# Kernel optimization log

Hardware: AMD Instinct MI355X
Metric: run time of the kernel (lower is better)

The kernel has to match this reference:

```python
import jax, jax.numpy as jnp
import numpy as np

N_NODES = 50000
N_EDGES = 800000


def _inv_sqrt_deg(idx, n):
    deg = jax.ops.segment_sum(jnp.ones(idx.shape, jnp.float32), idx, num_segments=n)
    return jnp.where(deg > 0, deg ** -0.5, 0.0)


def graph_conv(x, W, b, src, dst, norm_src, norm_dst):
    # DGL GraphConv, norm='both': D_dst^{-1/2} A D_src^{-1/2} X W + b
    # Apply weight before aggregation (out_feats < in_feats in both layers).
    h = (x * norm_src[:, None]) @ W            # [N, out]
    m = h[src]                                  # gather per-edge messages [E, out]
    agg = jax.ops.segment_sum(m, dst, num_segments=x.shape[0])
    return agg * norm_dst[:, None] + b


def setup_inputs() -> dict:
    key = jax.random.key(0)
    ks = jax.random.split(key, 6)
    x = jax.random.normal(ks[0], (N_NODES, 512), jnp.float32)
    W1 = jax.random.normal(ks[1], (512, 128), jnp.float32) * (512 ** -0.5)
    b1 = jnp.zeros((128,), jnp.float32)
    W2 = jax.random.normal(ks[2], (128, 40), jnp.float32) * (128 ** -0.5)
    b2 = jnp.zeros((40,), jnp.float32)
    src = jax.random.randint(ks[3], (N_EDGES,), 0, N_NODES, jnp.int32)
    dst = jax.random.randint(ks[4], (N_EDGES,), 0, N_NODES, jnp.int32)
    return {"x": x, "W1": W1, "b1": b1, "W2": W2, "b2": b2, "src": src, "dst": dst}


def reference(x, W1, b1, W2, b2, src, dst):
    n = x.shape[0]
    norm_src = _inv_sqrt_deg(src, n)  # out-degree based src norm
    norm_dst = _inv_sqrt_deg(dst, n)  # in-degree based dst norm
    h = graph_conv(x, W1, b1, src, dst, norm_src, norm_dst)
    h = jax.nn.relu(h)
    h = graph_conv(h, W2, b2, src, dst, norm_src, norm_dst)
    return h
```

## Files before the change

kernel.cpp:

```cpp
#include <hip/hip_runtime.h>
#include <hip/hip_bf16.h>

#define F0 512
#define F1 128
#define F2 40

#define NRP 12800
#define G_SL 64

typedef __attribute__((ext_vector_type(8))) short bf16x8;
typedef __attribute__((ext_vector_type(4))) float f32x4;

__device__ inline ushort f2bf(float f) {
    union { float f; uint u; } v; v.f = f;
    uint u = v.u;
    uint r = u + 0x7fffu + ((u >> 16) & 1u);
    return (ushort)(r >> 16);
}
__device__ inline float bf2f(ushort h) {
    union { uint u; float f; } v; v.u = ((uint)h) << 16;
    return v.f;
}

__global__ __launch_bounds__(1024)
void hist_kernel(const int* __restrict__ src, const int* __restrict__ dst,
                 ushort* __restrict__ Gsrc, ushort* __restrict__ Gdst, int n, int E) {
    __shared__ uint cs[NRP / 2];
    __shared__ uint cd[NRP / 2];
    const int p = blockIdx.x / G_SL;
    const int g = blockIdx.x % G_SL;
    const int base = p * NRP;
    for (int i = threadIdx.x; i < NRP / 2; i += 1024) { cs[i] = 0; cd[i] = 0; }
    __syncthreads();
    const int Epg = (E + G_SL - 1) / G_SL;
    const int e0 = g * Epg;
    const int e1 = min(E, e0 + Epg);
    for (int i = e0 + (int)threadIdx.x; i < e1; i += 1024) {
        int s = src[i], d = dst[i];
        unsigned so = (unsigned)(s - base);
        unsigned dd = (unsigned)(d - base);
        if (so < (unsigned)NRP) atomicAdd(&cs[so >> 1], 1u << ((so & 1) * 16));
        if (dd < (unsigned)NRP) atomicAdd(&cd[dd >> 1], 1u << ((dd & 1) * 16));
    }
    __syncthreads();
    const int lim = min(NRP, n - base);
    for (int i = threadIdx.x; i < lim; i += 1024) {
        uint pcs = cs[i >> 1], pcd = cd[i >> 1];
        int sh = (i & 1) * 16;
        Gsrc[(size_t)g * n + base + i] = (ushort)((pcs >> sh) & 0xffffu);
        Gdst[(size_t)g * n + base + i] = (ushort)((pcd >> sh) & 0xffffu);
    }
}

__global__ __launch_bounds__(256)
void scanA_kernel(const ushort* __restrict__ Gsrc, const ushort* __restrict__ Gdst,
                  float* __restrict__ norm_src, float* __restrict__ norm_dst,
                  int* __restrict__ row_off, int* __restrict__ bsum, int n) {
    __shared__ int sm[256];
    int i = blockIdx.x * 256 + threadIdx.x;
    int s = 0, d = 0;
    if (i < n) {
#pragma unroll
        for (int g = 0; g < G_SL; g++) {
            s += Gsrc[(size_t)g * n + i];
            d += Gdst[(size_t)g * n + i];
        }
        norm_src[i] = s > 0 ? rsqrtf((float)s) : 0.f;
        norm_dst[i] = d > 0 ? rsqrtf((float)d) : 0.f;
    }
    sm[threadIdx.x] = (i < n) ? d : 0;
    __syncthreads();
    for (int off = 1; off < 256; off <<= 1) {
        int t = (threadIdx.x >= (unsigned)off) ? sm[threadIdx.x - off] : 0;
        __syncthreads();
        sm[threadIdx.x] += t;
        __syncthreads();
    }
    if (i < n) row_off[i + 1] = sm[threadIdx.x];
    if (threadIdx.x == 255) bsum[blockIdx.x] = sm[255];
}

__global__ __launch_bounds__(256)
void finalize_kernel(int* __restrict__ row_off, const int* __restrict__ bsum,
                     const ushort* __restrict__ Gdst, int* __restrict__ Goff, int n) {
    __shared__ int sm[256];
    const int b = blockIdx.x;
    const int t = threadIdx.x;
    sm[t] = (t < b) ? bsum[t] : 0;
    __syncthreads();
#pragma unroll
    for (int off = 128; off > 0; off >>= 1) {
        if (t < off) sm[t] += sm[t + off];
        __syncthreads();
    }
    const int excl = sm[0];
    const int v = b * 256 + t;
    if (v >= n) return;
    int raw = row_off[v];
    int start = excl + ((t == 0) ? 0 : raw);
    if (v == n - 1) {
        int rawn = row_off[n];
        row_off[n] = excl + rawn;
    }
    row_off[v] = start;
    int run = start;
#pragma unroll
    for (int g = 0; g < G_SL; g++) {
        size_t idx = (size_t)g * n + v;
        Goff[idx] = run;
        run += Gdst[idx];
    }
}

__global__ __launch_bounds__(1024)
void place_kernel(const int* __restrict__ src, const int* __restrict__ dst,
                  const int* __restrict__ Goff, int* __restrict__ edge_src, int n, int E) {
    __shared__ int cur[NRP];
    const int p = blockIdx.x / G_SL;
    const int g = blockIdx.x % G_SL;
    const int base = p * NRP;
    const int lim = min(NRP, n - base);
    for (int i = threadIdx.x; i < lim; i += 1024)
        cur[i] = Goff[(size_t)g * n + base + i];
    __syncthreads();
    const int Epg = (E + G_SL - 1) / G_SL;
    const int e0 = g * Epg;
    const int e1 = min(E, e0 + Epg);
    for (int i = e0 + (int)threadIdx.x; i < e1; i += 1024) {
        int d = dst[i];
        unsigned dd = (unsigned)(d - base);
        if (dd < (unsigned)lim) {
            int pos = atomicAdd(&cur[dd], 1);
            edge_src[pos] = src[i];
        }
    }
}

__global__ __launch_bounds__(256)
void wconv1_kernel(const float* __restrict__ W1, ushort* __restrict__ Wt_hi) {
    int idx = blockIdx.x * 256 + threadIdx.x;
    int k = idx >> 7, nn = idx & 127;
    Wt_hi[nn * F0 + k] = f2bf(W1[idx]);
}

#define BM 64
__global__ __launch_bounds__(256)
void gemm1_mfma(const float* __restrict__ x, const ushort* __restrict__ Wt_hi,
                const float* __restrict__ norm_src, ushort* __restrict__ h1g, int n) {
    __shared__ __align__(16) ushort Al[2][4][2][64][8];

    const int tid = threadIdx.x;
    const int lane = tid & 63;
    const int w = tid >> 6;
    const int l15 = lane & 15;
    const int lq = lane >> 4;
    const int bm = blockIdx.x * BM;

    const int smi = tid >> 6;
    const int sflane = tid & 63;
    const int srow = smi * 16 + (tid & 15);
    const int skc = (tid >> 4) & 3;
    const int grow = bm + srow;
    const bool arok = grow < n;
    const float* xrow = x + (size_t)(arok ? grow : 0) * F0 + skc * 8;

    const size_t bgoff0 = (size_t)((w * 2 + 0) * 16 + l15) * F0 + lq * 8;
    const size_t bgoff1 = (size_t)((w * 2 + 1) * 16 + l15) * F0 + lq * 8;

    f32x4 acc[4][2] = {};
    float4 a0, a1;
    bf16x8 bcur0, bcur1, bnxt0, bnxt1;

    auto loadA = [&](int k0) {
        if (arok) {
            a0 = *reinterpret_cast<const float4*>(xrow + k0);
            a1 = *reinterpret_cast<const float4*>(xrow + k0 + 4);
        } else {
            a0 = make_float4(0.f, 0.f, 0.f, 0.f);
            a1 = a0;
        }
    };
    auto stageA = [&](int buf) {
        float cf[8] = {a0.x, a0.y, a0.z, a0.w, a1.x, a1.y, a1.z, a1.w};
        uint hu[4], lu[4];
#pragma unroll
        for (int j = 0; j < 4; j++) {
            float fa = cf[2 * j], fb = cf[2 * j + 1];
            __hip_bfloat162 h2 = __float22bfloat162_rn(make_float2(fa, fb));
            uint h; __builtin_memcpy(&h, &h2, 4);
            float ra = __uint_as_float(h << 16);
            float rb = __uint_as_float(h & 0xffff0000u);
            __hip_bfloat162 l2 = __float22bfloat162_rn(make_float2(fa - ra, fb - rb));
            uint l; __builtin_memcpy(&l, &l2, 4);
            hu[j] = h; lu[j] = l;
        }
        *reinterpret_cast<uint4*>(&Al[buf][smi][0][sflane][0]) = make_uint4(hu[0], hu[1], hu[2], hu[3]);
        *reinterpret_cast<uint4*>(&Al[buf][smi][1][sflane][0]) = make_uint4(lu[0], lu[1], lu[2], lu[3]);
    };
    auto compute = [&](int buf, bf16x8 b0, bf16x8 b1) {
#pragma unroll
        for (int mi = 0; mi < 4; mi++) {
            bf16x8 ah = *reinterpret_cast<const bf16x8*>(&Al[buf][mi][0][lane][0]);
            bf16x8 al = *reinterpret_cast<const bf16x8*>(&Al[buf][mi][1][lane][0]);
            acc[mi][0] = __builtin_amdgcn_mfma_f32_16x16x32_bf16(ah, b0, acc[mi][0], 0, 0, 0);
            acc[mi][0] = __builtin_amdgcn_mfma_f32_16x16x32_bf16(al, b0, acc[mi][0], 0, 0, 0);
            acc[mi][1] = __builtin_amdgcn_mfma_f32_16x16x32_bf16(ah, b1, acc[mi][1], 0, 0, 0);
            acc[mi][1] = __builtin_amdgcn_mfma_f32_16x16x32_bf16(al, b1, acc[mi][1], 0, 0, 0);
        }
    };

    loadA(0);
    bcur0 = *reinterpret_cast<const bf16x8*>(Wt_hi + bgoff0);
    bcur1 = *reinterpret_cast<const bf16x8*>(Wt_hi + bgoff1);
    stageA(0);
    __syncthreads();

    for (int kt = 0; kt < 16; kt++) {
        const int cb = kt & 1;
        if (kt < 15) {
            loadA((kt + 1) * 32);
            bnxt0 = *reinterpret_cast<const bf16x8*>(Wt_hi + bgoff0 + (kt + 1) * 32);
            bnxt1 = *reinterpret_cast<const bf16x8*>(Wt_hi + bgoff1 + (kt + 1) * 32);
        }
        compute(cb, bcur0, bcur1);
        if (kt < 15) {
            stageA(cb ^ 1);
            bcur0 = bnxt0; bcur1 = bnxt1;
            __syncthreads();
        }
    }

#pragma unroll
    for (int mi = 0; mi < 4; mi++) {
        int rbase = bm + mi * 16 + lq * 4;
#pragma unroll
        for (int r = 0; r < 4; r++) {
            int row = rbase + r;
            if (row < n) {
                float ns = norm_src[row];
#pragma unroll
                for (int ni = 0; ni < 2; ni++) {
                    h1g[(size_t)row * F1 + w * 32 + ni * 16 + l15] = f2bf(acc[mi][ni][r] * ns);
                }
            }
        }
    }
}

__global__ __launch_bounds__(256)
void agg1_kernel(const ushort* __restrict__ h1g, const int* __restrict__ row_off,
                 const int* __restrict__ edge_src, const float* __restrict__ norm_dst,
                 const float* __restrict__ b1, ushort* __restrict__ h1, int n) {
    int wid = (blockIdx.x * blockDim.x + threadIdx.x) >> 6;
    int lane = threadIdx.x & 63;
    if (wid >= n) return;
    int beg = row_off[wid], end = row_off[wid + 1];
    float a0 = 0.f, a1 = 0.f;
    int e = beg;
    for (; e + 3 < end; e += 4) {
        int s0 = edge_src[e + 0];
        int s1 = edge_src[e + 1];
        int s2 = edge_src[e + 2];
        int s3 = edge_src[e + 3];
        uint v0 = *reinterpret_cast<const uint*>(&h1g[(size_t)s0 * F1 + lane * 2]);
        uint v1 = *reinterpret_cast<const uint*>(&h1g[(size_t)s1 * F1 + lane * 2]);
        uint v2 = *reinterpret_cast<const uint*>(&h1g[(size_t)s2 * F1 + lane * 2]);
        uint v3 = *reinterpret_cast<const uint*>(&h1g[(size_t)s3 * F1 + lane * 2]);
        a0 += (__uint_as_float(v0 << 16) + __uint_as_float(v1 << 16)) +
              (__uint_as_float(v2 << 16) + __uint_as_float(v3 << 16));
        a1 += (__uint_as_float(v0 & 0xffff0000u) + __uint_as_float(v1 & 0xffff0000u)) +
              (__uint_as_float(v2 & 0xffff0000u) + __uint_as_float(v3 & 0xffff0000u));
    }
    for (; e < end; ++e) {
        int s = edge_src[e];
        uint v = *reinterpret_cast<const uint*>(&h1g[(size_t)s * F1 + lane * 2]);
        a0 += __uint_as_float(v << 16);
        a1 += __uint_as_float(v & 0xffff0000u);
    }
    float nd = norm_dst[wid];
    float o0 = fmaxf(a0 * nd + b1[lane * 2 + 0], 0.f);
    float o1 = fmaxf(a1 * nd + b1[lane * 2 + 1], 0.f);
    __hip_bfloat162 p2 = __float22bfloat162_rn(make_float2(o0, o1));
    uint pu; __builtin_memcpy(&pu, &p2, 4);
    *reinterpret_cast<uint*>(&h1[(size_t)wid * F1 + lane * 2]) = pu;
}

__global__ __launch_bounds__(256)
void gemm2_kernel(const ushort* __restrict__ h1, const float* __restrict__ W2,
                  const float* __restrict__ norm_src, ushort* __restrict__ h2g, int n) {
    __shared__ __align__(16) float W2s[F1][F2];
    for (int i = threadIdx.x; i < F1 * F2; i += 256)
        W2s[i / F2][i % F2] = W2[i];
    __syncthreads();
    int node = blockIdx.x * 256 + threadIdx.x;
    if (node >= n) return;
    float nrm = norm_src[node];
    f32x4 acc4[10] = {};
    const ushort* row = &h1[(size_t)node * F1];
    for (int kc = 0; kc < 16; kc++) {
        uint4 u = *reinterpret_cast<const uint4*>(&row[kc * 8]);
        uint uu[4] = {u.x, u.y, u.z, u.w};
        float f[8];
#pragma unroll
        for (int i = 0; i < 4; i++) {
            f[2 * i + 0] = __uint_as_float(uu[i] << 16);
            f[2 * i + 1] = __uint_as_float(uu[i] & 0xffff0000u);
        }
#pragma unroll
        for (int j = 0; j < 8; j++) {
#pragma unroll
            for (int c4 = 0; c4 < 10; c4++) {
                f32x4 wv = *reinterpret_cast<const f32x4*>(&W2s[kc * 8 + j][c4 * 4]);
                acc4[c4] += f[j] * wv;
            }
        }
    }
    ushort* orow = &h2g[(size_t)node * F2];
#pragma unroll
    for (int c4 = 0; c4 < 10; c4++) {
        f32x4 o = acc4[c4] * nrm;
        __hip_bfloat162 pa = __float22bfloat162_rn(make_float2(o[0], o[1]));
        __hip_bfloat162 pb = __float22bfloat162_rn(make_float2(o[2], o[3]));
        uint2 pk;
        __builtin_memcpy(&pk.x, &pa, 4);
        __builtin_memcpy(&pk.y, &pb, 4);
        *reinterpret_cast<uint2*>(&orow[c4 * 4]) = pk;
    }
}

__global__ __launch_bounds__(256)
void agg2_kernel(const ushort* __restrict__ h2g, const int* __restrict__ row_off,
                 const int* __restrict__ edge_src, const float* __restrict__ norm_dst,
                 const float* __restrict__ b2, float* __restrict__ out, int n) {
    int wid = (blockIdx.x * blockDim.x + threadIdx.x) >> 6;
    int lane = threadIdx.x & 63;
    if (wid >= n) return;
    int beg = row_off[wid], end = row_off[wid + 1];
    float a0 = 0.f, a1 = 0.f, b0 = 0.f, b1v = 0.f;
    int e = beg;
    const bool act = lane < 20;
    for (; e + 3 < end; e += 4) {
        int s0 = edge_src[e + 0];
        int s1 = edge_src[e + 1];
        int s2 = edge_src[e + 2];
        int s3 = edge_src[e + 3];
        if (act) {
            uint v0 = *reinterpret_cast<const uint*>(&h2g[(size_t)s0 * F2 + lane * 2]);
            uint v1 = *reinterpret_cast<const uint*>(&h2g[(size_t)s1 * F2 + lane * 2]);
            uint v2 = *reinterpret_cast<const uint*>(&h2g[(size_t)s2 * F2 + lane * 2]);
            uint v3 = *reinterpret_cast<const uint*>(&h2g[(size_t)s3 * F2 + lane * 2]);
            a0 += (__uint_as_float(v0 << 16) + __uint_as_float(v1 << 16)) +
                  (__uint_as_float(v2 << 16) + __uint_as_float(v3 << 16));
            b0 += (__uint_as_float(v0 & 0xffff0000u) + __uint_as_float(v1 & 0xffff0000u)) +
                  (__uint_as_float(v2 & 0xffff0000u) + __uint_as_float(v3 & 0xffff0000u));
        }
    }
    for (; e < end; ++e) {
        int s = edge_src[e];
        if (act) {
            uint v = *reinterpret_cast<const uint*>(&h2g[(size_t)s * F2 + lane * 2]);
            a1 += __uint_as_float(v << 16);
            b1v += __uint_as_float(v & 0xffff0000u);
        }
    }
    if (act) {
        float nd = norm_dst[wid];
        float o0 = (a0 + a1) * nd + b2[lane * 2 + 0];
        float o1 = (b0 + b1v) * nd + b2[lane * 2 + 1];
        *reinterpret_cast<float2*>(&out[(size_t)wid * F2 + lane * 2]) = make_float2(o0, o1);
    }
}

extern "C" void kernel_launch(void* const* d_in, const int* in_sizes, int n_in,
                              void* d_out, int out_size, void* d_ws, size_t ws_size,
                              hipStream_t stream) {
    const float* x  = (const float*)d_in[0];
    const float* W1 = (const float*)d_in[1];
    const float* b1 = (const float*)d_in[2];
    const float* W2 = (const float*)d_in[3];
    const float* b2 = (const float*)d_in[4];
    const int* src  = (const int*)d_in[5];
    const int* dst  = (const int*)d_in[6];
    float* out = (float*)d_out;

    const int n = in_sizes[0] / F0;
    const int E = in_sizes[5];
    const int nb = (n + 255) / 256;
    const int P = (n + NRP - 1) / NRP;

    char* ws = (char*)d_ws;
    auto alloc = [&](size_t bytes) -> char* {
        char* p = ws;
        ws += (bytes + 255) & ~(size_t)255;
        return p;
    };
    int* row_off   = (int*)alloc((size_t)(n + 1) * 4);
    int* bsum      = (int*)alloc(256 * 4);
    int* edge_srcs = (int*)alloc((size_t)E * 4);
    float* norm_src_d = (float*)alloc((size_t)n * 4);
    float* norm_dst_d = (float*)alloc((size_t)n * 4);
    ushort* W1t_hi = (ushort*)alloc((size_t)F1 * F0 * 2);
    ushort* h1g = (ushort*)alloc((size_t)n * F1 * 2);
    ushort* h1  = (ushort*)alloc((size_t)n * F1 * 2);
    ushort* h2g = h1g;

    ushort* Gsrc = (ushort*)h1g;
    ushort* Gdst = Gsrc + (size_t)G_SL * n;
    int* Goff = (int*)h1;

    hist_kernel<<<P * G_SL, 1024, 0, stream>>>(src, dst, Gsrc, Gdst, n, E);
    scanA_kernel<<<nb, 256, 0, stream>>>(Gsrc, Gdst, norm_src_d, norm_dst_d, row_off, bsum, n);
    finalize_kernel<<<nb, 256, 0, stream>>>(row_off, bsum, Gdst, Goff, n);
    place_kernel<<<P * G_SL, 1024, 0, stream>>>(src, dst, Goff, edge_srcs, n, E);
    wconv1_kernel<<<(F0 * F1) / 256, 256, 0, stream>>>(W1, W1t_hi);
    gemm1_mfma<<<(n + BM - 1) / BM, 256, 0, stream>>>(x, W1t_hi, norm_src_d, h1g, n);
    agg1_kernel<<<(n + 3) / 4, 256, 0, stream>>>(h1g, row_off, edge_srcs, norm_dst_d, b1, h1, n);
    gemm2_kernel<<<(n + 255) / 256, 256, 0, stream>>>(h1, W2, norm_src_d, h2g, n);
    agg2_kernel<<<(n + 3) / 4, 256, 0, stream>>>(h2g, row_off, edge_srcs, norm_dst_d, b2, out, n);
}
```

Before: 195.0 us.

## Drop split-bf16 GEMM1, fuse W1 convert into histogram, deepen prefetch and gather unroll

```diff
diff --git a/kernel.cpp b/kernel.cpp
--- a/kernel.cpp
+++ b/kernel.cpp
@@ -17,14 +17,16 @@
     uint r = u + 0x7fffu + ((u >> 16) & 1u);
     return (ushort)(r >> 16);
 }
-__device__ inline float bf2f(ushort h) {
-    union { uint u; float f; } v; v.u = ((uint)h) << 16;
-    return v.f;
-}
 
 __global__ __launch_bounds__(1024)
 void hist_kernel(const int* __restrict__ src, const int* __restrict__ dst,
-                 ushort* __restrict__ Gsrc, ushort* __restrict__ Gdst, int n, int E) {
+                 ushort* __restrict__ Gsrc, ushort* __restrict__ Gdst,
+                 const float* __restrict__ W1, ushort* __restrict__ Wt, int n, int E) {
+    if (blockIdx.x < (F0 * F1) / 1024) {
+        int idx = blockIdx.x * 1024 + threadIdx.x;
+        int k = idx >> 7, nn = idx & 127;
+        Wt[nn * F0 + k] = f2bf(W1[idx]);
+    }
     __shared__ uint cs[NRP / 2];
     __shared__ uint cd[NRP / 2];
     const int p = blockIdx.x / G_SL;
@@ -136,18 +138,11 @@
     }
 }
 
-__global__ __launch_bounds__(256)
-void wconv1_kernel(const float* __restrict__ W1, ushort* __restrict__ Wt_hi) {
-    int idx = blockIdx.x * 256 + threadIdx.x;
-    int k = idx >> 7, nn = idx & 127;
-    Wt_hi[nn * F0 + k] = f2bf(W1[idx]);
-}
-
 #define BM 64
 __global__ __launch_bounds__(256)
-void gemm1_mfma(const float* __restrict__ x, const ushort* __restrict__ Wt_hi,
+void gemm1_mfma(const float* __restrict__ x, const ushort* __restrict__ Wt,
                 const float* __restrict__ norm_src, ushort* __restrict__ h1g, int n) {
-    __shared__ __align__(16) ushort Al[2][4][2][64][8];
+    __shared__ __align__(16) ushort Al[2][4][64][8];
 
     const int tid = threadIdx.x;
     const int lane = tid & 63;
@@ -164,67 +159,67 @@
     const bool arok = grow < n;
     const float* xrow = x + (size_t)(arok ? grow : 0) * F0 + skc * 8;
 
-    const size_t bgoff0 = (size_t)((w * 2 + 0) * 16 + l15) * F0 + lq * 8;
-    const size_t bgoff1 = (size_t)((w * 2 + 1) * 16 + l15) * F0 + lq * 8;
+    const size_t bg0 = (size_t)((w * 2 + 0) * 16 + l15) * F0 + lq * 8;
+    const size_t bg1 = (size_t)((w * 2 + 1) * 16 + l15) * F0 + lq * 8;
 
     f32x4 acc[4][2] = {};
-    float4 a0, a1;
+    float4 sa0, sa1;
+    float4 sb0, sb1;
     bf16x8 bcur0, bcur1, bnxt0, bnxt1;
 
-    auto loadA = [&](int k0) {
+    auto loadA_A = [&](int k0) {
         if (arok) {
-            a0 = *reinterpret_cast<const float4*>(xrow + k0);
-            a1 = *reinterpret_cast<const float4*>(xrow + k0 + 4);
-        } else {
-            a0 = make_float4(0.f, 0.f, 0.f, 0.f);
-            a1 = a0;
-        }
-    };
-    auto stageA = [&](int buf) {
-        float cf[8] = {a0.x, a0.y, a0.z, a0.w, a1.x, a1.y, a1.z, a1.w};
-        uint hu[4], lu[4];
+            sa0 = *reinterpret_cast<const float4*>(xrow + k0);
+            sa1 = *reinterpret_cast<const float4*>(xrow + k0 + 4);
+        } else { sa0 = make_float4(0.f, 0.f, 0.f, 0.f); sa1 = sa0; }
+    };
+    auto loadA_B = [&](int k0) {
+        if (arok) {
+            sb0 = *reinterpret_cast<const float4*>(xrow + k0);
+            sb1 = *reinterpret_cast<const float4*>(xrow + k0 + 4);
+        } else { sb0 = make_float4(0.f, 0.f, 0.f, 0.f); sb1 = sb0; }
+    };
+    auto stage = [&](int buf, const float4& c0, const float4& c1) {
+        float cf[8] = {c0.x, c0.y, c0.z, c0.w, c1.x, c1.y, c1.z, c1.w};
+        uint hu[4];
 #pragma unroll
         for (int j = 0; j < 4; j++) {
-            float fa = cf[2 * j], fb = cf[2 * j + 1];
-            __hip_bfloat162 h2 = __float22bfloat162_rn(make_float2(fa, fb));
-            uint h; __builtin_memcpy(&h, &h2, 4);
-            float ra = __uint_as_float(h << 16);
-            float rb = __uint_as_float(h & 0xffff0000u);
-            __hip_bfloat162 l2 = __float22bfloat162_rn(make_float2(fa - ra, fb - rb));
-            uint l; __builtin_memcpy(&l, &l2, 4);
-            hu[j] = h; lu[j] = l;
-        }
-        *reinterpret_cast<uint4*>(&Al[buf][smi][0][sflane][0]) = make_uint4(hu[0], hu[1], hu[2], hu[3]);
-        *reinterpret_cast<uint4*>(&Al[buf][smi][1][sflane][0]) = make_uint4(lu[0], lu[1], lu[2], lu[3]);
+            __hip_bfloat162 h2 = __float22bfloat162_rn(make_float2(cf[2 * j], cf[2 * j + 1]));
+            __builtin_memcpy(&hu[j], &h2, 4);
+        }
+        *reinterpret_cast<uint4*>(&Al[buf][smi][sflane][0]) = make_uint4(hu[0], hu[1], hu[2], hu[3]);
+    };
+    auto loadB = [&](int k0, bf16x8& b0, bf16x8& b1) {
+        b0 = *reinterpret_cast<const bf16x8*>(Wt + bg0 + k0);
+        b1 = *reinterpret_cast<const bf16x8*>(Wt + bg1 + k0);
     };
     auto compute = [&](int buf, bf16x8 b0, bf16x8 b1) {
 #pragma unroll
         for (int mi = 0; mi < 4; mi++) {
-            bf16x8 ah = *reinterpret_cast<const bf16x8*>(&Al[buf][mi][0][lane][0]);
-            bf16x8 al = *reinterpret_cast<const bf16x8*>(&Al[buf][mi][1][lane][0]);
-            acc[mi][0] = __builtin_amdgcn_mfma_f32_16x16x32_bf16(ah, b0, acc[mi][0], 0, 0, 0);
-            acc[mi][0] = __builtin_amdgcn_mfma_f32_16x16x32_bf16(al, b0, acc[mi][0], 0, 0, 0);
-            acc[mi][1] = __builtin_amdgcn_mfma_f32_16x16x32_bf16(ah, b1, acc[mi][1], 0, 0, 0);
-            acc[mi][1] = __builtin_amdgcn_mfma_f32_16x16x32_bf16(al, b1, acc[mi][1], 0, 0, 0);
-        }
-    };
-
-    loadA(0);
-    bcur0 = *reinterpret_cast<const bf16x8*>(Wt_hi + bgoff0);
-    bcur1 = *reinterpret_cast<const bf16x8*>(Wt_hi + bgoff1);
-    stageA(0);
-    __syncthreads();
-
+            bf16x8 a = *reinterpret_cast<const bf16x8*>(&Al[buf][mi][lane][0]);
+            acc[mi][0] = __builtin_amdgcn_mfma_f32_16x16x32_bf16(a, b0, acc[mi][0], 0, 0, 0);
+            acc[mi][1] = __builtin_amdgcn_mfma_f32_16x16x32_bf16(a, b1, acc[mi][1], 0, 0, 0);
+        }
+    };
+
+    loadA_A(0);
+    loadA_B(32);
+    loadB(0, bcur0, bcur1);
+    stage(0, sa0, sa1);
+    __syncthreads();
+
+#pragma unroll
     for (int kt = 0; kt < 16; kt++) {
         const int cb = kt & 1;
-        if (kt < 15) {
-            loadA((kt + 1) * 32);
-            bnxt0 = *reinterpret_cast<const bf16x8*>(Wt_hi + bgoff0 + (kt + 1) * 32);
-            bnxt1 = *reinterpret_cast<const bf16x8*>(Wt_hi + bgoff1 + (kt + 1) * 32);
-        }
+        if (kt < 14) {
+            if ((kt & 1) == 0) loadA_A((kt + 2) * 32);
+            else               loadA_B((kt + 2) * 32);
+        }
+        if (kt < 15) loadB((kt + 1) * 32, bnxt0, bnxt1);
         compute(cb, bcur0, bcur1);
         if (kt < 15) {
-            stageA(cb ^ 1);
+            if (((kt + 1) & 1) == 0) stage(cb ^ 1, sa0, sa1);
+            else                     stage(cb ^ 1, sb0, sb1);
             bcur0 = bnxt0; bcur1 = bnxt1;
             __syncthreads();
         }
@@ -257,19 +252,19 @@
     int beg = row_off[wid], end = row_off[wid + 1];
     float a0 = 0.f, a1 = 0.f;
     int e = beg;
-    for (; e + 3 < end; e += 4) {
-        int s0 = edge_src[e + 0];
-        int s1 = edge_src[e + 1];
-        int s2 = edge_src[e + 2];
-        int s3 = edge_src[e + 3];
-        uint v0 = *reinterpret_cast<const uint*>(&h1g[(size_t)s0 * F1 + lane * 2]);
-        uint v1 = *reinterpret_cast<const uint*>(&h1g[(size_t)s1 * F1 + lane * 2]);
-        uint v2 = *reinterpret_cast<const uint*>(&h1g[(size_t)s2 * F1 + lane * 2]);
-        uint v3 = *reinterpret_cast<const uint*>(&h1g[(size_t)s3 * F1 + lane * 2]);
-        a0 += (__uint_as_float(v0 << 16) + __uint_as_float(v1 << 16)) +
-              (__uint_as_float(v2 << 16) + __uint_as_float(v3 << 16));
-        a1 += (__uint_as_float(v0 & 0xffff0000u) + __uint_as_float(v1 & 0xffff0000u)) +
-              (__uint_as_float(v2 & 0xffff0000u) + __uint_as_float(v3 & 0xffff0000u));
+    for (; e + 7 < end; e += 8) {
+        int s[8];
+#pragma unroll
+        for (int j = 0; j < 8; j++) s[j] = edge_src[e + j];
+        uint v[8];
+#pragma unroll
+        for (int j = 0; j < 8; j++)
+            v[j] = *reinterpret_cast<const uint*>(&h1g[(size_t)s[j] * F1 + lane * 2]);
+#pragma unroll
+        for (int j = 0; j < 8; j++) {
+            a0 += __uint_as_float(v[j] << 16);
+            a1 += __uint_as_float(v[j] & 0xffff0000u);
+        }
     }
     for (; e < end; ++e) {
         int s = edge_src[e];
@@ -336,37 +331,37 @@
     int lane = threadIdx.x & 63;
     if (wid >= n) return;
     int beg = row_off[wid], end = row_off[wid + 1];
-    float a0 = 0.f, a1 = 0.f, b0 = 0.f, b1v = 0.f;
+    float a0 = 0.f, a1 = 0.f;
     int e = beg;
     const bool act = lane < 20;
-    for (; e + 3 < end; e += 4) {
-        int s0 = edge_src[e + 0];
-        int s1 = edge_src[e + 1];
-        int s2 = edge_src[e + 2];
-        int s3 = edge_src[e + 3];
+    for (; e + 7 < end; e += 8) {
+        int s[8];
+#pragma unroll
+        for (int j = 0; j < 8; j++) s[j] = edge_src[e + j];
         if (act) {
-            uint v0 = *reinterpret_cast<const uint*>(&h2g[(size_t)s0 * F2 + lane * 2]);
-            uint v1 = *reinterpret_cast<const uint*>(&h2g[(size_t)s1 * F2 + lane * 2]);
-            uint v2 = *reinterpret_cast<const uint*>(&h2g[(size_t)s2 * F2 + lane * 2]);
-            uint v3 = *reinterpret_cast<const uint*>(&h2g[(size_t)s3 * F2 + lane * 2]);
-            a0 += (__uint_as_float(v0 << 16) + __uint_as_float(v1 << 16)) +
-                  (__uint_as_float(v2 << 16) + __uint_as_float(v3 << 16));
-            b0 += (__uint_as_float(v0 & 0xffff0000u) + __uint_as_float(v1 & 0xffff0000u)) +
-                  (__uint_as_float(v2 & 0xffff0000u) + __uint_as_float(v3 & 0xffff0000u));
+            uint v[8];
+#pragma unroll
+            for (int j = 0; j < 8; j++)
+                v[j] = *reinterpret_cast<const uint*>(&h2g[(size_t)s[j] * F2 + lane * 2]);
+#pragma unroll
+            for (int j = 0; j < 8; j++) {
+                a0 += __uint_as_float(v[j] << 16);
+                a1 += __uint_as_float(v[j] & 0xffff0000u);
+            }
         }
     }
     for (; e < end; ++e) {
         int s = edge_src[e];
         if (act) {
             uint v = *reinterpret_cast<const uint*>(&h2g[(size_t)s * F2 + lane * 2]);
-            a1 += __uint_as_float(v << 16);
-            b1v += __uint_as_float(v & 0xffff0000u);
+            a0 += __uint_as_float(v << 16);
+            a1 += __uint_as_float(v & 0xffff0000u);
         }
     }
     if (act) {
         float nd = norm_dst[wid];
-        float o0 = (a0 + a1) * nd + b2[lane * 2 + 0];
-        float o1 = (b0 + b1v) * nd + b2[lane * 2 + 1];
+        float o0 = a0 * nd + b2[lane * 2 + 0];
+        float o1 = a1 * nd + b2[lane * 2 + 1];
         *reinterpret_cast<float2*>(&out[(size_t)wid * F2 + lane * 2]) = make_float2(o0, o1);
     }
 }
@@ -399,7 +394,7 @@
     int* edge_srcs = (int*)alloc((size_t)E * 4);
     float* norm_src_d = (float*)alloc((size_t)n * 4);
     float* norm_dst_d = (float*)alloc((size_t)n * 4);
-    ushort* W1t_hi = (ushort*)alloc((size_t)F1 * F0 * 2);
+    ushort* W1t = (ushort*)alloc((size_t)F1 * F0 * 2);
     ushort* h1g = (ushort*)alloc((size_t)n * F1 * 2);
     ushort* h1  = (ushort*)alloc((size_t)n * F1 * 2);
     ushort* h2g = h1g;
@@ -408,12 +403,11 @@
     ushort* Gdst = Gsrc + (size_t)G_SL * n;
     int* Goff = (int*)h1;
 
-    hist_kernel<<<P * G_SL, 1024, 0, stream>>>(src, dst, Gsrc, Gdst, n, E);
+    hist_kernel<<<P * G_SL, 1024, 0, stream>>>(src, dst, Gsrc, Gdst, W1, W1t, n, E);
     scanA_kernel<<<nb, 256, 0, stream>>>(Gsrc, Gdst, norm_src_d, norm_dst_d, row_off, bsum, n);
     finalize_kernel<<<nb, 256, 0, stream>>>(row_off, bsum, Gdst, Goff, n);
     place_kernel<<<P * G_SL, 1024, 0, stream>>>(src, dst, Goff, edge_srcs, n, E);
-    wconv1_kernel<<<(F0 * F1) / 256, 256, 0, stream>>>(W1, W1t_hi);
-    gemm1_mfma<<<(n + BM - 1) / BM, 256, 0, stream>>>(x, W1t_hi, norm_src_d, h1g, n);
+    gemm1_mfma<<<(n + BM - 1) / BM, 256, 0, stream>>>(x, W1t, norm_src_d, h1g, n);
     agg1_kernel<<<(n + 3) / 4, 256, 0, stream>>>(h1g, row_off, edge_srcs, norm_dst_d, b1, h1, n);
     gemm2_kernel<<<(n + 255) / 256, 256, 0, stream>>>(h1, W2, norm_src_d, h2g, n);
     agg2_kernel<<<(n + 3) / 4, 256, 0, stream>>>(h2g, row_off, edge_srcs, norm_dst_d, b2, out, n);
```

After: 192.5 us. About the same (-1.3%).
